# Kernel tuning notes

Measured on AMD Instinct MI355X. Metric: run time of the kernel, lower is better.

Reference implementation:

```python
import jax, jax.numpy as jnp
import numpy as np
from jax import lax
from jax.scipy.special import logsumexp

LOG2PI = 1.8378770664093453

def _gauss_lp(x, mean, logvar):
    return -0.5 * ((x - mean) ** 2 * jnp.exp(-logvar) + logvar + LOG2PI)

def setup_inputs() -> dict:
    key = jax.random.key(0)
    ks = jax.random.split(key, 12)
    B, T, D, H, X, K, U = 32, 1024, 512, 512, 32, 8, 2
    s = 0.05
    return {
        'ys': jax.random.normal(ks[0], (B, T, D), jnp.float32),
        'us': jax.random.normal(ks[1], (B, T, U), jnp.float32),
        'eps': jax.random.normal(ks[2], (B, T, X), jnp.float32),
        'W1': jax.random.normal(ks[3], (D, H), jnp.float32) * s,
        'b1': jnp.zeros((H,), jnp.float32),
        'Wmu': jax.random.normal(ks[4], (H, X), jnp.float32) * s,
        'bmu': jnp.zeros((X,), jnp.float32),
        'Wlv': jax.random.normal(ks[5], (H, X), jnp.float32) * s,
        'blv': jnp.zeros((X,), jnp.float32),
        'Wz': jax.random.normal(ks[6], (X, K * K), jnp.float32) * s,
        'bz': jnp.zeros((K * K,), jnp.float32),
        'A': jax.random.normal(ks[7], (K, X, X), jnp.float32) * s,
        'Bu': jax.random.normal(ks[8], (K, U, X), jnp.float32) * s,
        'bx': jnp.zeros((K, X), jnp.float32),
        'x_logvar': jnp.zeros((K, X), jnp.float32),
        'x0_mean': jax.random.normal(ks[9], (K, X), jnp.float32) * s,
        'x0_logvar': jnp.zeros((K, X), jnp.float32),
        'C': jax.random.normal(ks[10], (X, D), jnp.float32) * s,
        'd': jnp.zeros((D,), jnp.float32),
        'y_logvar': jnp.zeros((D,), jnp.float32),
        'log_init_z': jnp.zeros((K,), jnp.float32),
    }

def _forward_backward(log_a, log_b, log_init):
    # log_a: [B,T,K,K] with log_a[:,t,j,k] = log p(z_t=j | z_{t-1}=k); log_b: [B,T,K]
    B, T, K = log_b.shape
    la = jnp.moveaxis(log_a[:, 1:], 1, 0)  # [T-1,B,K,K]
    lb = jnp.moveaxis(log_b[:, 1:], 1, 0)  # [T-1,B,K]
    a0 = log_init[None, :] + log_b[:, 0]
    c0 = logsumexp(a0, axis=-1)
    a0 = a0 - c0[:, None]
    def fstep(alpha, ab):
        la_t, lb_t = ab
        a = lb_t + logsumexp(la_t + alpha[:, None, :], axis=-1)
        c = logsumexp(a, axis=-1)
        an = a - c[:, None]
        return an, (an, c)
    _, (alphas, cs) = lax.scan(fstep, a0, (la, lb))
    log_px = c0 + jnp.sum(cs, axis=0)  # [B] log marginal likelihood
    fwd = jnp.concatenate([a0[None], alphas], axis=0)  # [T,B,K]
    betaT = jnp.zeros((B, K), log_b.dtype)
    def bstep(beta, ab):
        la_t, lb_t = ab
        b = logsumexp(la_t + (lb_t + beta)[:, :, None], axis=1)  # sum over next-state j
        b = b - logsumexp(b, axis=-1, keepdims=True)
        return b, b
    _, betas = lax.scan(bstep, betaT, (la, lb), reverse=True)
    bwd = jnp.concatenate([betas, betaT[None]], axis=0)  # [T,B,K]
    lg = fwd + bwd
    log_gamma1 = lg - logsumexp(lg, axis=-1, keepdims=True)
    return jnp.moveaxis(log_gamma1, 0, 1), log_px

def reference(ys, us, eps, W1, b1, Wmu, bmu, Wlv, blv, Wz, bz, A, Bu, bx,
              x_logvar, x0_mean, x0_logvar, C, d, y_logvar, log_init_z):
    B, T, D = ys.shape
    K, X = x0_mean.shape
    # inference net q(x|y): per-step MLP producing Gaussian, reparameterized sample
    h = jnp.tanh(ys @ W1 + b1)
    mu = h @ Wmu + bmu
    lv = h @ Wlv + blv
    x = mu + jnp.exp(0.5 * lv) * eps                        # [B,T,X]
    x_entropy = 0.5 * jnp.sum(eps ** 2 + lv + LOG2PI, -1)   # -log q(x^), [B,T]
    # discrete transition log p(z_t | z_{t-1}, x_{t-1}) with log(eye) prepended at t=0
    logits = (x[:, :-1] @ Wz + bz).reshape(B, T - 1, K, K)
    log_a_t = jax.nn.log_softmax(logits, axis=-2)           # normalize_logprob axis=-2
    log_eye = jnp.log(jnp.eye(K, dtype=ys.dtype) + 1e-10)[None, None]
    log_a = jnp.concatenate([jnp.broadcast_to(log_eye, (B, 1, K, K)), log_a_t], axis=1)
    # continuous likelihood log p(x_t | x_{t-1}, u_t, z_t=k) -> [B,T,K]
    log_b0 = jnp.sum(_gauss_lp(x[:, 0, None, :], x0_mean, x0_logvar), -1)  # [B,K]
    means = (jnp.einsum('btd,kde->btke', x[:, :-1], A)
             + jnp.einsum('btu,kue->btke', us[:, 1:], Bu) + bx)            # [B,T-1,K,X]
    log_bt = jnp.sum(_gauss_lp(x[:, 1:, None, :], means, x_logvar), -1)
    log_b = jnp.concatenate([log_b0[:, None], log_bt], axis=1)
    log_init = jax.nn.log_softmax(log_init_z)
    log_gamma1, log_px = _forward_backward(log_a, log_b, log_init)
    # posterior-weighted generated mean mixed over states, then emission
    xt1_gen = jnp.sum(means * jnp.exp(log_gamma1[:, 1:, :, None]), axis=-2)
    x_gen1 = jnp.concatenate([x[:, :1], xt1_gen], axis=1)
    y_mean = x_gen1 @ C + d
    log_py = jnp.sum(_gauss_lp(ys, y_mean, y_logvar), -1)   # [B,T]
    log_p_xy = log_px + jnp.sum(log_py, -1)                 # [B]
    log_qx = jnp.mean(jnp.sum(x_entropy, 1))
    elbo = jnp.mean(log_p_xy) + log_qx
    return elbo
```

## Files before the change

### kernel.cpp

```cpp
#include <hip/hip_runtime.h>
#include <math.h>

#define LOG2PI 1.8378770664093453f

#define NB 32
#define NT 1024
#define ND 512
#define NH 512
#define NX 32
#define NK 8
#define NU 2

#define NCH 93
#define CHL 11

typedef __attribute__((ext_vector_type(8))) short bf16x8;
typedef __attribute__((ext_vector_type(4))) float f32x4;

__device__ __forceinline__ unsigned short f2bf(float f) {
    unsigned u = __float_as_uint(f);
    unsigned r = (u + 0x7FFF + ((u >> 16) & 1)) >> 16;
    return (unsigned short)r;
}

#define DPP_X1 0xB1
#define DPP_X2 0x4E
#define DPP_X3 0x1B
#define DPP_X7 0x141

template <int CTRL>
__device__ __forceinline__ float dppx(float v) {
    return __int_as_float(__builtin_amdgcn_update_dpp(
        0, __float_as_int(v), CTRL, 0xF, 0xF, true));
}

__device__ __forceinline__ float fb_matvec(float4 a0, float4 a1, float v) {
    float p1 = dppx<DPP_X1>(v);
    float p2 = dppx<DPP_X2>(v);
    float p3 = dppx<DPP_X3>(v);
    float p7 = dppx<DPP_X7>(v);
    float p4 = dppx<DPP_X7>(p3);
    float p5 = dppx<DPP_X7>(p2);
    float p6 = dppx<DPP_X7>(p1);
    float c0 = fmaf(a0.y, p1, a0.x * v);
    float c1 = fmaf(a0.w, p3, a0.z * p2);
    float c2 = fmaf(a1.y, p5, a1.x * p4);
    float c3 = fmaf(a1.w, p7, a1.z * p6);
    return (c0 + c1) + (c2 + c3);
}

__device__ __forceinline__ float fb_matvecT(float4 a0, float4 a1, float w) {
    float q0 = a0.x * w;
    float t1 = dppx<DPP_X1>(a0.y * w);
    float t2 = dppx<DPP_X2>(a0.z * w);
    float t3 = dppx<DPP_X3>(a0.w * w);
    float t7 = dppx<DPP_X7>(a1.w * w);
    float t4 = dppx<DPP_X7>(dppx<DPP_X3>(a1.x * w));
    float t5 = dppx<DPP_X7>(dppx<DPP_X2>(a1.y * w));
    float t6 = dppx<DPP_X7>(dppx<DPP_X1>(a1.z * w));
    return ((q0 + t1) + (t2 + t3)) + ((t4 + t5) + (t6 + t7));
}

__device__ __forceinline__ float gsum8(float v) {
    float s = v + dppx<DPP_X1>(v);
    s = s + dppx<DPP_X2>(s);
    s = s + dppx<DPP_X7>(dppx<DPP_X3>(s));
    return s;
}

__device__ __forceinline__ float lse8_high(float v) {
    float m = v;
    m = fmaxf(m, __shfl_xor(m, 8, 64));
    m = fmaxf(m, __shfl_xor(m, 16, 64));
    m = fmaxf(m, __shfl_xor(m, 32, 64));
    float s = expf(v - m);
    s += __shfl_xor(s, 8, 64);
    s += __shfl_xor(s, 16, 64);
    s += __shfl_xor(s, 32, 64);
    return m + logf(s);
}

__global__ __launch_bounds__(256) void k_castT(
    const float* __restrict__ W, unsigned short* __restrict__ WT)
{
    __shared__ float tile[32][33];
    const int bx = blockIdx.x * 32;
    const int by = blockIdx.y * 32;
    const int tx = threadIdx.x & 31, ty = threadIdx.x >> 5;
    for (int i = ty; i < 32; i += 8)
        tile[i][tx] = W[(size_t)(bx + i) * 512 + by + tx];
    __syncthreads();
    for (int i = ty; i < 32; i += 8)
        WT[(size_t)(by + i) * 512 + bx + tx] = f2bf(tile[tx][i]);
}

__global__ __launch_bounds__(256) void k_cast_mulv(
    const float* __restrict__ Wmu, const float* __restrict__ Wlv,
    unsigned short* __restrict__ out)
{
    __shared__ float tile[32][33];
    const float* W = blockIdx.y ? Wlv : Wmu;
    const int base = blockIdx.y * 32;
    const int g = blockIdx.x;
    const int tx = threadIdx.x & 31, ty = threadIdx.x >> 5;
    for (int i = ty; i < 32; i += 8)
        tile[i][tx] = W[(size_t)(g * 32 + i) * 32 + tx];
    __syncthreads();
    for (int i = ty; i < 32; i += 8)
        out[(size_t)(base + i) * 512 + g * 32 + tx] = f2bf(tile[tx][i]);
}

__global__ __launch_bounds__(256) void k_prepc1(
    const float* __restrict__ ylv, float* __restrict__ ivbuf,
    float* __restrict__ term0)
{
    __shared__ float part[256];
    const int tid = threadIdx.x;
    float s = 0.f;
    for (int i = tid; i < 512; i += 256) {
        float lv = ylv[i];
        ivbuf[i] = expf(-lv);
        s += lv + LOG2PI;
    }
    part[tid] = s;
    __syncthreads();
    for (int st = 128; st; st >>= 1) {
        if (tid < st) part[tid] += part[tid + st];
        __syncthreads();
    }
    if (tid == 0) term0[0] = part[0];
}

__global__ __launch_bounds__(256) void k_prepc2(
    const float* __restrict__ C, const float* __restrict__ dvec,
    const float* __restrict__ ivbuf, unsigned short* __restrict__ W2bf,
    float* __restrict__ G, float* __restrict__ c2x)
{
    const int x = blockIdx.x;
    const int tid = threadIdx.x;
    if (x == 32) {
        for (int i = tid; i < 32 * 512; i += 256)
            W2bf[i] = f2bf(C[i] * ivbuf[i & 511]);
        return;
    }
    const int y = tid >> 3, seg = tid & 7;
    const float* Cx = &C[(size_t)x * 512];
    const float* Cy = &C[(size_t)y * 512];
    float p = 0.f;
    for (int j = 0; j < 64; ++j) {
        int dcol = seg * 64 + j;
        p = fmaf(Cx[dcol] * ivbuf[dcol], Cy[dcol], p);
    }
    p = gsum8(p);
    if (seg == 0) G[x * 33 + y] = p;
    if (tid < 8) {
        float q = 0.f;
        for (int j = 0; j < 64; ++j) {
            int dcol = tid * 64 + j;
            q = fmaf(Cx[dcol] * ivbuf[dcol], dvec[dcol], q);
        }
        q = gsum8(q);
        if (tid == 0) c2x[x] = q;
    }
}

__global__ __launch_bounds__(256) void k_gemm_h_mfma(
    const float* __restrict__ ys,
    const unsigned short* __restrict__ Bbf,
    const float* __restrict__ b1, unsigned short* __restrict__ hb)
{
    __shared__ unsigned short As[128 * 64];
    __shared__ unsigned short Bs[128 * 64];
    const int tid = threadIdx.x;
    const int bm = blockIdx.y * 128;
    const int bn = blockIdx.x * 128;
    const int wid = tid >> 6, lane = tid & 63;
    const int wm = wid >> 1, wn = wid & 1;

    f32x4 acc[4][4];
#pragma unroll
    for (int m = 0; m < 4; ++m)
#pragma unroll
        for (int n = 0; n < 4; ++n)
            acc[m][n] = (f32x4){0.f, 0.f, 0.f, 0.f};

    for (int k0 = 0; k0 < 512; k0 += 64) {
#pragma unroll
        for (int r = 0; r < 4; ++r) {
            int l = tid + r * 256;
            int row = l >> 3, c8 = l & 7;
            int sidx = row * 8 + (c8 ^ (row & 7));
            const float4 f0 = *reinterpret_cast<const float4*>(
                &ys[(size_t)(bm + row) * 512 + k0 + c8 * 8]);
            const float4 f1 = *reinterpret_cast<const float4*>(
                &ys[(size_t)(bm + row) * 512 + k0 + c8 * 8 + 4]);
            uint4 ua;
            ua.x = (unsigned)f2bf(f0.x) | ((unsigned)f2bf(f0.y) << 16);
            ua.y = (unsigned)f2bf(f0.z) | ((unsigned)f2bf(f0.w) << 16);
            ua.z = (unsigned)f2bf(f1.x) | ((unsigned)f2bf(f1.y) << 16);
            ua.w = (unsigned)f2bf(f1.z) | ((unsigned)f2bf(f1.w) << 16);
            *reinterpret_cast<uint4*>(&As[sidx * 8]) = ua;
            uint4 vb = *reinterpret_cast<const uint4*>(
                &Bbf[(size_t)(bn + row) * 512 + k0 + c8 * 8]);
            *reinterpret_cast<uint4*>(&Bs[sidx * 8]) = vb;
        }
        __syncthreads();
#pragma unroll
        for (int kh = 0; kh < 2; ++kh) {
            bf16x8 af[4], bfr[4];
            const int c8r = kh * 4 + (lane >> 4);
#pragma unroll
            for (int m = 0; m < 4; ++m) {
                int rA = wm * 64 + m * 16 + (lane & 15);
                af[m] = *reinterpret_cast<bf16x8*>(
                    &As[rA * 64 + (c8r ^ (rA & 7)) * 8]);
            }
#pragma unroll
            for (int n = 0; n < 4; ++n) {
                int rB = wn * 64 + n * 16 + (lane & 15);
                bfr[n] = *reinterpret_cast<bf16x8*>(
                    &Bs[rB * 64 + (c8r ^ (rB & 7)) * 8]);
            }
#pragma unroll
            for (int m = 0; m < 4; ++m)
#pragma unroll
                for (int n = 0; n < 4; ++n)
                    acc[m][n] = __builtin_amdgcn_mfma_f32_16x16x32_bf16(
                        af[m], bfr[n], acc[m][n], 0, 0, 0);
        }
        __syncthreads();
    }
    float b1v[4];
#pragma unroll
    for (int n = 0; n < 4; ++n)
        b1v[n] = b1[bn + wn * 64 + n * 16 + (lane & 15)];
#pragma unroll
    for (int m = 0; m < 4; ++m) {
#pragma unroll
        for (int q = 0; q < 4; ++q) {
            int row = bm + wm * 64 + m * 16 + (lane >> 4) * 4 + q;
#pragma unroll
            for (int n = 0; n < 4; ++n) {
                int col = bn + wn * 64 + n * 16 + (lane & 15);
                hb[(size_t)row * 512 + col] = f2bf(tanhf(acc[m][n][q] + b1v[n]));
            }
        }
    }
}

__global__ __launch_bounds__(256) void k_mulv_mfma(
    const unsigned short* __restrict__ hbf,
    const unsigned short* __restrict__ Wt,
    const float* __restrict__ bmu, const float* __restrict__ blv,
    const float* __restrict__ eps,
    float* __restrict__ x, float* __restrict__ xent)
{
    __shared__ unsigned short As[128 * 64];
    __shared__ unsigned short Bs[64 * 64];
    const int tid = threadIdx.x;
    const int bm = blockIdx.x * 128;
    const int wid = tid >> 6, lane = tid & 63;
    f32x4 acc[2][4];
#pragma unroll
    for (int m = 0; m < 2; ++m)
#pragma unroll
        for (int n = 0; n < 4; ++n)
            acc[m][n] = (f32x4){0.f, 0.f, 0.f, 0.f};

    for (int k0 = 0; k0 < 512; k0 += 64) {
#pragma unroll
        for (int r = 0; r < 4; ++r) {
            int l = tid + r * 256, row = l >> 3, c8 = l & 7;
            int sidx = row * 8 + (c8 ^ (row & 7));
            uint4 v = *reinterpret_cast<const uint4*>(
                &hbf[(size_t)(bm + row) * 512 + k0 + c8 * 8]);
            *reinterpret_cast<uint4*>(&As[sidx * 8]) = v;
        }
#pragma unroll
        for (int r = 0; r < 2; ++r) {
            int l = tid + r * 256, row = l >> 3, c8 = l & 7;
            int sidx = row * 8 + (c8 ^ (row & 7));
            uint4 v = *reinterpret_cast<const uint4*>(
                &Wt[(size_t)row * 512 + k0 + c8 * 8]);
            *reinterpret_cast<uint4*>(&Bs[sidx * 8]) = v;
        }
        __syncthreads();
#pragma unroll
        for (int kh = 0; kh < 2; ++kh) {
            const int c8r = kh * 4 + (lane >> 4);
            bf16x8 af[2], bfr[4];
#pragma unroll
            for (int m = 0; m < 2; ++m) {
                int rA = wid * 32 + m * 16 + (lane & 15);
                af[m] = *reinterpret_cast<bf16x8*>(
                    &As[rA * 64 + (c8r ^ (rA & 7)) * 8]);
            }
#pragma unroll
            for (int n = 0; n < 4; ++n) {
                int rB = n * 16 + (lane & 15);
                bfr[n] = *reinterpret_cast<bf16x8*>(
                    &Bs[rB * 64 + (c8r ^ (rB & 7)) * 8]);
            }
#pragma unroll
            for (int m = 0; m < 2; ++m)
#pragma unroll
                for (int n = 0; n < 4; ++n)
                    acc[m][n] = __builtin_amdgcn_mfma_f32_16x16x32_bf16(
                        af[m], bfr[n], acc[m][n], 0, 0, 0);
        }
        __syncthreads();
    }
    const int o0 = lane & 15, o1 = 16 + (lane & 15);
    const float bm0 = bmu[o0], bm1 = bmu[o1];
    const float bl0 = blv[o0], bl1 = blv[o1];
#pragma unroll
    for (int m = 0; m < 2; ++m) {
#pragma unroll
        for (int q = 0; q < 4; ++q) {
            int row = bm + wid * 32 + m * 16 + (lane >> 4) * 4 + q;
            float mu0 = acc[m][0][q] + bm0;
            float mu1 = acc[m][1][q] + bm1;
            float lv0 = acc[m][2][q] + bl0;
            float lv1 = acc[m][3][q] + bl1;
            float e0 = eps[(size_t)row * 32 + o0];
            float e1 = eps[(size_t)row * 32 + o1];
            x[(size_t)row * 32 + o0] = mu0 + expf(0.5f * lv0) * e0;
            x[(size_t)row * 32 + o1] = mu1 + expf(0.5f * lv1) * e1;
            float pe = (e0 * e0 + lv0) + (e1 * e1 + lv1);
            pe += __shfl_xor(pe, 1, 64);
            pe += __shfl_xor(pe, 2, 64);
            pe += __shfl_xor(pe, 4, 64);
            pe += __shfl_xor(pe, 8, 64);
            if ((lane & 15) == 0)
                xent[row] = 0.5f * (pe + 32.f * LOG2PI);
        }
    }
}

__global__ __launch_bounds__(256) void k_proj(
    const float* __restrict__ ys, const unsigned short* __restrict__ W2bf,
    const float* __restrict__ dvec, const float* __restrict__ ivbuf,
    float* __restrict__ proj, float* __restrict__ term1)
{
    __shared__ unsigned short As[128 * 64];
    __shared__ unsigned short Bs[32 * 64];
    const int tid = threadIdx.x;
    const int bm = blockIdx.x * 128;
    const int wid = tid >> 6, lane = tid & 63;
    const int c8 = tid & 7;
    f32x4 acc[2][2];
#pragma unroll
    for (int m = 0; m < 2; ++m)
#pragma unroll
        for (int n = 0; n < 2; ++n)
            acc[m][n] = (f32x4){0.f, 0.f, 0.f, 0.f};
    float t1p[4] = {0.f, 0.f, 0.f, 0.f};

    for (int k0 = 0; k0 < 512; k0 += 64) {
        const float4 dv0 = *reinterpret_cast<const float4*>(&dvec[k0 + c8 * 8]);
        const float4 dv1 = *reinterpret_cast<const float4*>(&dvec[k0 + c8 * 8 + 4]);
        const float4 iv0 = *reinterpret_cast<const float4*>(&ivbuf[k0 + c8 * 8]);
        const float4 iv1 = *reinterpret_cast<const float4*>(&ivbuf[k0 + c8 * 8 + 4]);
#pragma unroll
        for (int r = 0; r < 4; ++r) {
            int l = tid + r * 256;
            int row = l >> 3;
            int sidx = row * 8 + (c8 ^ (row & 7));
            const float4 f0 = *reinterpret_cast<const float4*>(
                &ys[(size_t)(bm + row) * 512 + k0 + c8 * 8]);
            const float4 f1 = *reinterpret_cast<const float4*>(
                &ys[(size_t)(bm + row) * 512 + k0 + c8 * 8 + 4]);
            float g0 = f0.x - dv0.x, g1 = f0.y - dv0.y;
            float g2 = f0.z - dv0.z, g3 = f0.w - dv0.w;
            float g4 = f1.x - dv1.x, g5 = f1.y - dv1.y;
            float g6 = f1.z - dv1.z, g7 = f1.w - dv1.w;
            t1p[r] += (g0 * g0 * iv0.x + g1 * g1 * iv0.y)
                    + (g2 * g2 * iv0.z + g3 * g3 * iv0.w)
                    + (g4 * g4 * iv1.x + g5 * g5 * iv1.y)
                    + (g6 * g6 * iv1.z + g7 * g7 * iv1.w);
            uint4 ua;
            ua.x = (unsigned)f2bf(f0.x) | ((unsigned)f2bf(f0.y) << 16);
            ua.y = (unsigned)f2bf(f0.z) | ((unsigned)f2bf(f0.w) << 16);
            ua.z = (unsigned)f2bf(f1.x) | ((unsigned)f2bf(f1.y) << 16);
            ua.w = (unsigned)f2bf(f1.z) | ((unsigned)f2bf(f1.w) << 16);
            *reinterpret_cast<uint4*>(&As[sidx * 8]) = ua;
        }
        {
            int row = tid >> 3;
            int sidx = row * 8 + (c8 ^ (row & 7));
            uint4 v = *reinterpret_cast<const uint4*>(
                &W2bf[(size_t)row * 512 + k0 + c8 * 8]);
            *reinterpret_cast<uint4*>(&Bs[sidx * 8]) = v;
        }
        __syncthreads();
#pragma unroll
        for (int kh = 0; kh < 2; ++kh) {
            const int c8r = kh * 4 + (lane >> 4);
            bf16x8 af[2], bfr[2];
#pragma unroll
            for (int m = 0; m < 2; ++m) {
                int rA = wid * 32 + m * 16 + (lane & 15);
                af[m] = *reinterpret_cast<bf16x8*>(
                    &As[rA * 64 + (c8r ^ (rA & 7)) * 8]);
            }
#pragma unroll
            for (int n = 0; n < 2; ++n) {
                int rB = n * 16 + (lane & 15);
                bfr[n] = *reinterpret_cast<bf16x8*>(
                    &Bs[rB * 64 + (c8r ^ (rB & 7)) * 8]);
            }
#pragma unroll
            for (int m = 0; m < 2; ++m)
#pragma unroll
                for (int n = 0; n < 2; ++n)
                    acc[m][n] = __builtin_amdgcn_mfma_f32_16x16x32_bf16(
                        af[m], bfr[n], acc[m][n], 0, 0, 0);
        }
        __syncthreads();
    }
#pragma unroll
    for (int m = 0; m < 2; ++m)
#pragma unroll
        for (int q = 0; q < 4; ++q) {
            int row = bm + wid * 32 + m * 16 + (lane >> 4) * 4 + q;
#pragma unroll
            for (int n = 0; n < 2; ++n) {
                int col = n * 16 + (lane & 15);
                proj[(size_t)row * 32 + col] = acc[m][n][q];
            }
        }
#pragma unroll
    for (int r = 0; r < 4; ++r) {
        float s = gsum8(t1p[r]);
        if ((tid & 7) == 0) term1[bm + (tid >> 3) + r * 32] = s;
    }
}

__global__ __launch_bounds__(256) void k_loga(
    const float* __restrict__ x, const float* __restrict__ Wz,
    const float* __restrict__ bz, float* __restrict__ ap1)
{
    const int tid = threadIdx.x;
    const int item = blockIdx.x * 4 + (tid >> 6);
    const int lane = tid & 63;
    const int t = item & (NT - 1);
    if (t == 0) return;
    const int j = lane >> 3, k = lane & 7;
    const float* xr = &x[((size_t)item - 1) * 32];
    float acc = bz[lane];
#pragma unroll
    for (int e = 0; e < 32; ++e) acc = fmaf(xr[e], Wz[e * 64 + lane], acc);
    float lse = lse8_high(acc);
    ap1[(size_t)item * 64 + j * 8 + (j ^ k)] = expf(acc - lse);
}

__global__ __launch_bounds__(256) void k_means(
    const float* __restrict__ x, const float* __restrict__ us,
    const float* __restrict__ A, const float* __restrict__ Bu,
    const float* __restrict__ bx, const float* __restrict__ x_logvar,
    float* __restrict__ means, float* __restrict__ log_b)
{
    __shared__ float xs[32];
    __shared__ float uu[2];
    const int item = blockIdx.x;
    const int b = item / 1023;
    const int tm = item - b * 1023;
    const int tid = threadIdx.x;
    const int k = tid >> 5, xo = tid & 31;
    if (tid < 32) xs[tid] = x[((size_t)b * NT + tm) * 32 + tid];
    if (tid < 2) uu[tid] = us[((size_t)b * NT + tm + 1) * 2 + tid];
    __syncthreads();
    float acc = bx[k * 32 + xo];
#pragma unroll
    for (int e = 0; e < 32; ++e)
        acc = fmaf(xs[e], A[((size_t)k * 32 + e) * 32 + xo], acc);
    acc = fmaf(uu[0], Bu[((size_t)k * 2 + 0) * 32 + xo], acc);
    acc = fmaf(uu[1], Bu[((size_t)k * 2 + 1) * 32 + xo], acc);
    means[((size_t)item * 8 + k) * 32 + xo] = acc;
    float xv = x[((size_t)b * NT + tm + 1) * 32 + xo];
    float lvv = x_logvar[k * 32 + xo];
    float dd = xv - acc;
    float term = -0.5f * (dd * dd * expf(-lvv) + lvv + LOG2PI);
    for (int m = 16; m; m >>= 1) term += __shfl_down(term, m, 32);
    if (xo == 0) log_b[((size_t)b * NT + tm + 1) * 8 + k] = term;
}

__global__ __launch_bounds__(256) void k_logb0(
    const float* __restrict__ x, const float* __restrict__ x0_mean,
    const float* __restrict__ x0_logvar, float* __restrict__ log_b)
{
    const int b = blockIdx.x;
    const int tid = threadIdx.x;
    const int k = tid >> 5, xo = tid & 31;
    float xv = x[((size_t)b * NT) * 32 + xo];
    float mm = x0_mean[k * 32 + xo];
    float lvv = x0_logvar[k * 32 + xo];
    float dd = xv - mm;
    float term = -0.5f * (dd * dd * expf(-lvv) + lvv + LOG2PI);
    for (int m = 16; m; m >>= 1) term += __shfl_down(term, m, 32);
    if (xo == 0) log_b[(size_t)b * NT * 8 + k] = term;
}

__global__ __launch_bounds__(256) void k_prep(
    const float* __restrict__ log_b, float* __restrict__ bexp,
    float* __restrict__ mbsum)
{
    __shared__ float part[256];
    const int b = blockIdx.x;
    const int tid = threadIdx.x;
    float msum = 0.f;
    for (int t = tid; t < NT; t += 256) {
        const float* lbp = &log_b[((size_t)b * NT + t) * 8];
        float4 l0 = *reinterpret_cast<const float4*>(lbp);
        float4 l1 = *reinterpret_cast<const float4*>(lbp + 4);
        float mm = fmaxf(fmaxf(fmaxf(l0.x, l0.y), fmaxf(l0.z, l0.w)),
                         fmaxf(fmaxf(l1.x, l1.y), fmaxf(l1.z, l1.w)));
        float4 e0, e1;
        e0.x = expf(l0.x - mm); e0.y = expf(l0.y - mm);
        e0.z = expf(l0.z - mm); e0.w = expf(l0.w - mm);
        e1.x = expf(l1.x - mm); e1.y = expf(l1.y - mm);
        e1.z = expf(l1.z - mm); e1.w = expf(l1.w - mm);
        float* bp = &bexp[((size_t)b * NT + t) * 8];
        *reinterpret_cast<float4*>(bp) = e0;
        *reinterpret_cast<float4*>(bp + 4) = e1;
        msum += mm;
    }
    part[tid] = msum;
    __syncthreads();
    for (int s = 128; s; s >>= 1) {
        if (tid < s) part[tid] += part[tid + s];
        __syncthreads();
    }
    if (tid == 0) mbsum[b] = part[0];
}

__global__ __launch_bounds__(256) void k_fbA(
    const float* __restrict__ ap1, const float* __restrict__ bexp,
    float* __restrict__ Pfx, float* __restrict__ sA)
{
    const int tid = threadIdx.x;
    const int wg = blockIdx.x * 4 + (tid >> 6);
    const int lane = tid & 63;
    const int b = wg / NCH;
    const int c = wg - b * NCH;
    const int j = lane >> 3, k = lane & 7;
    const float* ap = &ap1[(size_t)b * NT * 64];
    const float* be = &bexp[(size_t)b * NT * 8];
    int t = CHL * c + 1;
    float P = be[t * 8 + j] * ap[t * 64 + j * 8 + (j ^ k)];
    float sacc = 0.f;
    for (int i = 1; i < CHL; ++i) {
        ++t;
        float4 m0 = *reinterpret_cast<const float4*>(&ap[(size_t)t * 64 + j * 8]);
        float4 m1 = *reinterpret_cast<const float4*>(&ap[(size_t)t * 64 + j * 8 + 4]);
        float bj = be[(size_t)t * 8 + j];
        float x1 = __shfl_xor(P, 8, 64);
        float x2 = __shfl_xor(P, 16, 64);
        float x3 = __shfl_xor(P, 24, 64);
        float x4 = __shfl_xor(P, 32, 64);
        float x5 = __shfl_xor(P, 40, 64);
        float x6 = __shfl_xor(P, 48, 64);
        float x7 = __shfl_xor(P, 56, 64);
        float c0 = fmaf(m0.y, x1, m0.x * P);
        float c1 = fmaf(m0.w, x3, m0.z * x2);
        float c2 = fmaf(m1.y, x5, m1.x * x4);
        float c3 = fmaf(m1.w, x7, m1.z * x6);
        P = bj * ((c0 + c1) + (c2 + c3));
        if ((i & 3) == 3) {
            float mx = P;
            mx = fmaxf(mx, __shfl_xor(mx, 1, 64));
            mx = fmaxf(mx, __shfl_xor(mx, 2, 64));
            mx = fmaxf(mx, __shfl_xor(mx, 4, 64));
            mx = fmaxf(mx, __shfl_xor(mx, 8, 64));
            mx = fmaxf(mx, __shfl_xor(mx, 16, 64));
            mx = fmaxf(mx, __shfl_xor(mx, 32, 64));
            mx = fmaxf(mx, 1e-30f);
            float r = __builtin_amdgcn_rcpf(mx);
            P *= r;
            sacc -= __logf(r);
        }
    }
    Pfx[((size_t)b * NCH + c) * 64 + j * 8 + (j ^ k)] = P;
    if (lane == 0) sA[b * NCH + c] = sacc;
}

__global__ __launch_bounds__(128) void k_fbB(
    const float* __restrict__ Pfx, const float* __restrict__ sA,
    const float* __restrict__ bexp, const float* __restrict__ mbsum,
    const float* __restrict__ log_init_z,
    float* __restrict__ alphaB, float* __restrict__ betaB,
    float* __restrict__ log_px)
{
    const int b = blockIdx.x;
    const int tid = threadIdx.x;
    const int wave = tid >> 6;
    const int lane = tid & 63;
    const int st = lane & 7;
    const float* pf = &Pfx[(size_t)b * NCH * 64];
    if (wave == 0) {
        float liv[8];
        float mz = -1e30f, sz = 0.f;
#pragma unroll
        for (int q = 0; q < 8; ++q) liv[q] = log_init_z[q];
#pragma unroll
        for (int q = 0; q < 8; ++q) mz = fmaxf(mz, liv[q]);
#pragma unroll
        for (int q = 0; q < 8; ++q) sz += expf(liv[q] - mz);
        float alpha = (expf(liv[st] - mz) / sz) * bexp[(size_t)b * NT * 8 + st];
        float logS = 0.f, sAsum = 0.f;
        {
            float s = fmaxf(gsum8(alpha), 1e-35f);
            logS += __logf(s);
            alpha *= __builtin_amdgcn_rcpf(s);
        }
        if (lane < 8) alphaB[((size_t)b * (NCH + 1)) * 8 + lane] = alpha;
        for (int c = 0; c < NCH; ++c) {
            float4 a0 = *reinterpret_cast<const float4*>(&pf[(size_t)c * 64 + st * 8]);
            float4 a1 = *reinterpret_cast<const float4*>(&pf[(size_t)c * 64 + st * 8 + 4]);
            alpha = fb_matvec(a0, a1, alpha);
            float s = fmaxf(gsum8(alpha), 1e-35f);
            logS += __logf(s);
            alpha *= __builtin_amdgcn_rcpf(s);
            sAsum += sA[b * NCH + c];
            if (lane < 8) alphaB[((size_t)b * (NCH + 1) + c + 1) * 8 + lane] = alpha;
        }
        if (lane == 0) log_px[b] = mbsum[b] + sAsum + logS;
    } else {
        float beta = 1.f;
        if (lane < 8) betaB[((size_t)b * (NCH + 1) + NCH) * 8 + lane] = 1.f;
        for (int c = NCH - 1; c >= 0; --c) {
            float4 a0 = *reinterpret_cast<const float4*>(&pf[(size_t)c * 64 + st * 8]);
            float4 a1 = *reinterpret_cast<const float4*>(&pf[(size_t)c * 64 + st * 8 + 4]);
            beta = fb_matvecT(a0, a1, beta);
            float s = fmaxf(gsum8(beta), 1e-35f);
            beta *= __builtin_amdgcn_rcpf(s);
            if (lane < 8) betaB[((size_t)b * (NCH + 1) + c) * 8 + lane] = beta;
        }
    }
}

__global__ __launch_bounds__(256) void k_fbC(
    const float* __restrict__ ap1, const float* __restrict__ bexp,
    const float* __restrict__ alphaB, const float* __restrict__ betaB,
    float* __restrict__ gamma)
{
    __shared__ float alphaS[32][CHL][8];
    const int tid = threadIdx.x;
    const int g = tid >> 3;
    const int st = tid & 7;
    const int task = blockIdx.x * 32 + g;
    const int b = task / NCH;
    const int c = task - b * NCH;
    const float* ap = &ap1[(size_t)b * NT * 64];
    const float* be = &bexp[(size_t)b * NT * 8];
    const int t0 = CHL * c;
    float alpha = alphaB[((size_t)b * (NCH + 1) + c) * 8 + st];
#pragma unroll
    for (int i = 1; i <= CHL; ++i) {
        int t = t0 + i;
        float4 a0 = *reinterpret_cast<const float4*>(&ap[(size_t)t * 64 + st * 8]);
        float4 a1 = *reinterpret_cast<const float4*>(&ap[(size_t)t * 64 + st * 8 + 4]);
        float bv = be[(size_t)t * 8 + st];
        alpha = fb_matvec(a0, a1, alpha) * bv;
        if (i == 5)
            alpha *= __builtin_amdgcn_rcpf(fmaxf(gsum8(alpha), 1e-35f));
        alphaS[g][i - 1][st] = alpha;
    }
    float beta = betaB[((size_t)b * (NCH + 1) + c + 1) * 8 + st];
#pragma unroll
    for (int i = CHL; i >= 1; --i) {
        int t = t0 + i;
        float gv = alphaS[g][i - 1][st] * beta;
        float s = fmaxf(gsum8(gv), 1e-35f);
        gamma[((size_t)b * NT + t) * 8 + st] = gv * __builtin_amdgcn_rcpf(s);
        float4 a0 = *reinterpret_cast<const float4*>(&ap[(size_t)t * 64 + st * 8]);
        float4 a1 = *reinterpret_cast<const float4*>(&ap[(size_t)t * 64 + st * 8 + 4]);
        float bv = be[(size_t)t * 8 + st];
        beta = fb_matvecT(a0, a1, beta * bv);
        if (i == 6)
            beta *= __builtin_amdgcn_rcpf(fmaxf(gsum8(beta), 1e-35f));
    }
    if (c == 0) {
        float a0v = alphaB[((size_t)b * (NCH + 1)) * 8 + st];
        float gv = a0v * beta;
        float s = fmaxf(gsum8(gv), 1e-35f);
        gamma[((size_t)b * NT) * 8 + st] = gv * __builtin_amdgcn_rcpf(s);
    }
}

__global__ __launch_bounds__(256) void k_py(
    const float* __restrict__ x, const float* __restrict__ means,
    const float* __restrict__ gamma, const float* __restrict__ proj,
    const float* __restrict__ term1, const float* __restrict__ Gm,
    const float* __restrict__ c2x, const float* __restrict__ term0,
    const float* __restrict__ xent, float* __restrict__ red)
{
    __shared__ float Gs[32 * 33];
    __shared__ float c2s[32];
    __shared__ float xgS[8][32];
    const int tid = threadIdx.x;
    const int itemBase = blockIdx.x * 8;
    const int b = itemBase >> 10;
    const int t0 = itemBase & (NT - 1);
    for (int i = tid; i < 32 * 33; i += 256) Gs[i] = Gm[i];
    if (tid < 32) c2s[tid] = c2x[tid];
    __syncthreads();
    const int it = tid >> 5;
    const int xo = tid & 31;
    const int t = t0 + it;
    const int item = itemBase + it;
    float xg;
    if (t == 0) {
        xg = x[(size_t)item * 32 + xo];
    } else {
        const float* gp = &gamma[(size_t)item * 8];
        const float* mp = &means[(((size_t)b * 1023 + (t - 1)) * 8) * 32 + xo];
        float4 g0 = *reinterpret_cast<const float4*>(gp);
        float4 g1 = *reinterpret_cast<const float4*>(gp + 4);
        xg = mp[0 * 32] * g0.x;
        xg = fmaf(mp[1 * 32], g0.y, xg);
        xg = fmaf(mp[2 * 32], g0.z, xg);
        xg = fmaf(mp[3 * 32], g0.w, xg);
        xg = fmaf(mp[4 * 32], g1.x, xg);
        xg = fmaf(mp[5 * 32], g1.y, xg);
        xg = fmaf(mp[6 * 32], g1.z, xg);
        xg = fmaf(mp[7 * 32], g1.w, xg);
    }
    xgS[it][xo] = xg;
    __syncthreads();
    float gmv = 0.f;
#pragma unroll 8
    for (int y = 0; y < 32; ++y)
        gmv = fmaf(Gs[xo * 33 + y], xgS[it][y], gmv);
    float val = xg * (proj[(size_t)item * 32 + xo] - c2s[xo] - 0.5f * gmv);
    val += __shfl_xor(val, 1, 64);
    val += __shfl_xor(val, 2, 64);
    val += __shfl_xor(val, 4, 64);
    val += __shfl_xor(val, 8, 64);
    val += __shfl_xor(val, 16, 64);
    if (xo == 0)
        red[item] = -0.5f * (term1[item] + term0[0]) + val + xent[item];
}

__global__ __launch_bounds__(256) void k_final(
    const float* __restrict__ red, const float* __restrict__ log_px,
    float* __restrict__ out)
{
    __shared__ float ssum[4];
    float s = 0.f;
    for (int i = threadIdx.x; i < NB * NT; i += 256) s += red[i];
    if (threadIdx.x < NB) s += log_px[threadIdx.x];
#pragma unroll
    for (int m = 1; m < 64; m <<= 1) s += __shfl_xor(s, m, 64);
    if ((threadIdx.x & 63) == 0) ssum[threadIdx.x >> 6] = s;
    __syncthreads();
    if (threadIdx.x == 0)
        out[0] = (ssum[0] + ssum[1] + ssum[2] + ssum[3]) / (float)NB;
}

extern "C" void kernel_launch(void* const* d_in, const int* in_sizes, int n_in,
                              void* d_out, int out_size, void* d_ws,
                              size_t ws_size, hipStream_t stream)
{
    const float* ys        = (const float*)d_in[0];
    const float* us        = (const float*)d_in[1];
    const float* eps       = (const float*)d_in[2];
    const float* W1        = (const float*)d_in[3];
    const float* b1        = (const float*)d_in[4];
    const float* Wmu       = (const float*)d_in[5];
    const float* bmu       = (const float*)d_in[6];
    const float* Wlv       = (const float*)d_in[7];
    const float* blv       = (const float*)d_in[8];
    const float* Wz        = (const float*)d_in[9];
    const float* bz        = (const float*)d_in[10];
    const float* A         = (const float*)d_in[11];
    const float* Bu        = (const float*)d_in[12];
    const float* bx        = (const float*)d_in[13];
    const float* x_logvar  = (const float*)d_in[14];
    const float* x0_mean   = (const float*)d_in[15];
    const float* x0_logvar = (const float*)d_in[16];
    const float* C         = (const float*)d_in[17];
    const float* dv        = (const float*)d_in[18];
    const float* y_logvar  = (const float*)d_in[19];
    const float* log_init_z= (const float*)d_in[20];
    float* out = (float*)d_out;

    float* ws = (float*)d_ws;
    float* hbf_f  = ws;
    float* x      = hbf_f + 8388608;
    float* xent   = x + 1048576;
    float* ap1    = xent + 32768;
    float* bexp   = ap1 + 2097152;
    float* log_b  = bexp + 262144;
    float* means  = log_b + 262144;
    float* gam    = means + 8380416;
    float* log_px = gam + 262144;
    float* mbsum  = log_px + 32;
    float* red    = mbsum + 32;
    float* w1t_f  = red + 32768;
    float* wmlv_f = w1t_f + 131072;
    float* proj   = wmlv_f + 16384;
    float* term1  = proj + 1048576;
    float* ivbuf  = term1 + 32768;
    float* w2bf_f = ivbuf + 512;
    float* Gm     = w2bf_f + 8192;
    float* c2x    = Gm + 1056;
    float* term0  = c2x + 32;
    float* Pfx    = term0 + 1;
    float* sA     = Pfx + 190464;
    float* alphaB = sA + 2976;
    float* betaB  = alphaB + 24064;

    unsigned short* hbf  = (unsigned short*)hbf_f;
    unsigned short* w1t  = (unsigned short*)w1t_f;
    unsigned short* wmlv = (unsigned short*)wmlv_f;
    unsigned short* w2bf = (unsigned short*)w2bf_f;

    k_castT    <<<dim3(16, 16), 256, 0, stream>>>(W1, w1t);
    k_cast_mulv<<<dim3(16, 2), 256, 0, stream>>>(Wmu, Wlv, wmlv);
    k_prepc1   <<<1, 256, 0, stream>>>(y_logvar, ivbuf, term0);
    k_prepc2   <<<33, 256, 0, stream>>>(C, dv, ivbuf, w2bf, Gm, c2x);
    k_gemm_h_mfma<<<dim3(4, 256), 256, 0, stream>>>(ys, w1t, b1, hbf);
    k_proj     <<<256, 256, 0, stream>>>(ys, w2bf, dv, ivbuf, proj, term1);
    k_mulv_mfma<<<256, 256, 0, stream>>>(hbf, wmlv, bmu, blv, eps, x, xent);
    k_loga <<<8192, 256, 0, stream>>>(x, Wz, bz, ap1);
    k_means<<<32 * 1023, 256, 0, stream>>>(x, us, A, Bu, bx, x_logvar, means, log_b);
    k_logb0<<<32, 256, 0, stream>>>(x, x0_mean, x0_logvar, log_b);
    k_prep <<<32, 256, 0, stream>>>(log_b, bexp, mbsum);
    k_fbA  <<<744, 256, 0, stream>>>(ap1, bexp, Pfx, sA);
    k_fbB  <<<32, 128, 0, stream>>>(Pfx, sA, bexp, mbsum, log_init_z,
                                    alphaB, betaB, log_px);
    k_fbC  <<<93, 256, 0, stream>>>(ap1, bexp, alphaB, betaB, gam);
    k_py   <<<4096, 256, 0, stream>>>(x, means, gam, proj, term1, Gm, c2x,
                                      term0, xent, red);
    k_final<<<1, 256, 0, stream>>>(red, log_px, out);
}
```

Measured before the change: 271.2 us.

## Precast ys to bf16 once, drop means buffer by recomputing in k_py

Adds a kernel that converts ys to bf16 and computes the term1 quadratic in one pass. Both GEMMs then read the compact bf16 copy instead of each re-reading and converting fp32 ys, and the h GEMM grid is swapped so row tiles vary fastest. The ~32MB means tensor is no longer written; k_means now batches 8 items per block with A staged in LDS and k_py recomputes the per-state means from A. This trades extra arithmetic and an extra bf16 write/read of ys for much less global memory traffic.

Result: slower. 283.0 us (+4.4%).

```diff
diff --git a/kernel.cpp b/kernel.cpp
--- a/kernel.cpp
+++ b/kernel.cpp
@@ -21,6 +21,12 @@
     unsigned u = __float_as_uint(f);
     unsigned r = (u + 0x7FFF + ((u >> 16) & 1)) >> 16;
     return (unsigned short)r;
+}
+
+__device__ __forceinline__ unsigned pack_bf2(float a, float b) {
+    unsigned ua = __float_as_uint(a) + 0x8000u;
+    unsigned ub = __float_as_uint(b) + 0x8000u;
+    return __builtin_amdgcn_perm(ub, ua, 0x07060302);
 }
 
 #define DPP_X1 0xB1
@@ -164,16 +170,60 @@
     }
 }
 
+__global__ __launch_bounds__(256) void k_cast_ys_t1(
+    const float* __restrict__ ys, const float* __restrict__ dvec,
+    const float* __restrict__ ivbuf, unsigned short* __restrict__ ysb,
+    float* __restrict__ term1)
+{
+    const int tid = threadIdx.x;
+    const int c8 = tid & 7;
+    const int rbase = blockIdx.x * 128;
+    float t1p[4] = {0.f, 0.f, 0.f, 0.f};
+    for (int k0 = 0; k0 < 512; k0 += 64) {
+        const float4 dv0 = *reinterpret_cast<const float4*>(&dvec[k0 + c8 * 8]);
+        const float4 dv1 = *reinterpret_cast<const float4*>(&dvec[k0 + c8 * 8 + 4]);
+        const float4 iv0 = *reinterpret_cast<const float4*>(&ivbuf[k0 + c8 * 8]);
+        const float4 iv1 = *reinterpret_cast<const float4*>(&ivbuf[k0 + c8 * 8 + 4]);
+#pragma unroll
+        for (int r = 0; r < 4; ++r) {
+            int row = rbase + (tid >> 3) + r * 32;
+            const float4 f0 = *reinterpret_cast<const float4*>(
+                &ys[(size_t)row * 512 + k0 + c8 * 8]);
+            const float4 f1 = *reinterpret_cast<const float4*>(
+                &ys[(size_t)row * 512 + k0 + c8 * 8 + 4]);
+            float g0 = f0.x - dv0.x, g1 = f0.y - dv0.y;
+            float g2 = f0.z - dv0.z, g3 = f0.w - dv0.w;
+            float g4 = f1.x - dv1.x, g5 = f1.y - dv1.y;
+            float g6 = f1.z - dv1.z, g7 = f1.w - dv1.w;
+            t1p[r] += (g0 * g0 * iv0.x + g1 * g1 * iv0.y)
+                    + (g2 * g2 * iv0.z + g3 * g3 * iv0.w)
+                    + (g4 * g4 * iv1.x + g5 * g5 * iv1.y)
+                    + (g6 * g6 * iv1.z + g7 * g7 * iv1.w);
+            uint4 ua;
+            ua.x = pack_bf2(f0.x, f0.y);
+            ua.y = pack_bf2(f0.z, f0.w);
+            ua.z = pack_bf2(f1.x, f1.y);
+            ua.w = pack_bf2(f1.z, f1.w);
+            *reinterpret_cast<uint4*>(&ysb[(size_t)row * 512 + k0 + c8 * 8]) = ua;
+        }
+    }
+#pragma unroll
+    for (int r = 0; r < 4; ++r) {
+        float s = gsum8(t1p[r]);
+        if ((tid & 7) == 0) term1[rbase + (tid >> 3) + r * 32] = s;
+    }
+}
+
 __global__ __launch_bounds__(256) void k_gemm_h_mfma(
-    const float* __restrict__ ys,
+    const unsigned short* __restrict__ Abf,
     const unsigned short* __restrict__ Bbf,
     const float* __restrict__ b1, unsigned short* __restrict__ hb)
 {
     __shared__ unsigned short As[128 * 64];
     __shared__ unsigned short Bs[128 * 64];
     const int tid = threadIdx.x;
-    const int bm = blockIdx.y * 128;
-    const int bn = blockIdx.x * 128;
+    const int bm = blockIdx.x * 128;
+    const int bn = blockIdx.y * 128;
     const int wid = tid >> 6, lane = tid & 63;
     const int wm = wid >> 1, wn = wid & 1;
 
@@ -190,16 +240,9 @@
             int l = tid + r * 256;
             int row = l >> 3, c8 = l & 7;
             int sidx = row * 8 + (c8 ^ (row & 7));
-            const float4 f0 = *reinterpret_cast<const float4*>(
-                &ys[(size_t)(bm + row) * 512 + k0 + c8 * 8]);
-            const float4 f1 = *reinterpret_cast<const float4*>(
-                &ys[(size_t)(bm + row) * 512 + k0 + c8 * 8 + 4]);
-            uint4 ua;
-            ua.x = (unsigned)f2bf(f0.x) | ((unsigned)f2bf(f0.y) << 16);
-            ua.y = (unsigned)f2bf(f0.z) | ((unsigned)f2bf(f0.w) << 16);
-            ua.z = (unsigned)f2bf(f1.x) | ((unsigned)f2bf(f1.y) << 16);
-            ua.w = (unsigned)f2bf(f1.z) | ((unsigned)f2bf(f1.w) << 16);
-            *reinterpret_cast<uint4*>(&As[sidx * 8]) = ua;
+            uint4 va = *reinterpret_cast<const uint4*>(
+                &Abf[(size_t)(bm + row) * 512 + k0 + c8 * 8]);
+            *reinterpret_cast<uint4*>(&As[sidx * 8]) = va;
             uint4 vb = *reinterpret_cast<const uint4*>(
                 &Bbf[(size_t)(bn + row) * 512 + k0 + c8 * 8]);
             *reinterpret_cast<uint4*>(&Bs[sidx * 8]) = vb;
@@ -338,55 +381,32 @@
 }
 
 __global__ __launch_bounds__(256) void k_proj(
-    const float* __restrict__ ys, const unsigned short* __restrict__ W2bf,
-    const float* __restrict__ dvec, const float* __restrict__ ivbuf,
-    float* __restrict__ proj, float* __restrict__ term1)
+    const unsigned short* __restrict__ ysb,
+    const unsigned short* __restrict__ W2bf, float* __restrict__ proj)
 {
     __shared__ unsigned short As[128 * 64];
     __shared__ unsigned short Bs[32 * 64];
     const int tid = threadIdx.x;
     const int bm = blockIdx.x * 128;
     const int wid = tid >> 6, lane = tid & 63;
-    const int c8 = tid & 7;
     f32x4 acc[2][2];
 #pragma unroll
     for (int m = 0; m < 2; ++m)
 #pragma unroll
         for (int n = 0; n < 2; ++n)
             acc[m][n] = (f32x4){0.f, 0.f, 0.f, 0.f};
-    float t1p[4] = {0.f, 0.f, 0.f, 0.f};
 
     for (int k0 = 0; k0 < 512; k0 += 64) {
-        const float4 dv0 = *reinterpret_cast<const float4*>(&dvec[k0 + c8 * 8]);
-        const float4 dv1 = *reinterpret_cast<const float4*>(&dvec[k0 + c8 * 8 + 4]);
-        const float4 iv0 = *reinterpret_cast<const float4*>(&ivbuf[k0 + c8 * 8]);
-        const float4 iv1 = *reinterpret_cast<const float4*>(&ivbuf[k0 + c8 * 8 + 4]);
 #pragma unroll
         for (int r = 0; r < 4; ++r) {
-            int l = tid + r * 256;
-            int row = l >> 3;
+            int l = tid + r * 256, row = l >> 3, c8 = l & 7;
             int sidx = row * 8 + (c8 ^ (row & 7));
-            const float4 f0 = *reinterpret_cast<const float4*>(
-                &ys[(size_t)(bm + row) * 512 + k0 + c8 * 8]);
-            const float4 f1 = *reinterpret_cast<const float4*>(
-                &ys[(size_t)(bm + row) * 512 + k0 + c8 * 8 + 4]);
-            float g0 = f0.x - dv0.x, g1 = f0.y - dv0.y;
-            float g2 = f0.z - dv0.z, g3 = f0.w - dv0.w;
-            float g4 = f1.x - dv1.x, g5 = f1.y - dv1.y;
-            float g6 = f1.z - dv1.z, g7 = f1.w - dv1.w;
-            t1p[r] += (g0 * g0 * iv0.x + g1 * g1 * iv0.y)
-                    + (g2 * g2 * iv0.z + g3 * g3 * iv0.w)
-                    + (g4 * g4 * iv1.x + g5 * g5 * iv1.y)
-                    + (g6 * g6 * iv1.z + g7 * g7 * iv1.w);
-            uint4 ua;
-            ua.x = (unsigned)f2bf(f0.x) | ((unsigned)f2bf(f0.y) << 16);
-            ua.y = (unsigned)f2bf(f0.z) | ((unsigned)f2bf(f0.w) << 16);
-            ua.z = (unsigned)f2bf(f1.x) | ((unsigned)f2bf(f1.y) << 16);
-            ua.w = (unsigned)f2bf(f1.z) | ((unsigned)f2bf(f1.w) << 16);
-            *reinterpret_cast<uint4*>(&As[sidx * 8]) = ua;
+            uint4 v = *reinterpret_cast<const uint4*>(
+                &ysb[(size_t)(bm + row) * 512 + k0 + c8 * 8]);
+            *reinterpret_cast<uint4*>(&As[sidx * 8]) = v;
         }
         {
-            int row = tid >> 3;
+            int row = tid >> 3, c8 = tid & 7;
             int sidx = row * 8 + (c8 ^ (row & 7));
             uint4 v = *reinterpret_cast<const uint4*>(
                 &W2bf[(size_t)row * 512 + k0 + c8 * 8]);
@@ -429,11 +449,6 @@
                 proj[(size_t)row * 32 + col] = acc[m][n][q];
             }
         }
-#pragma unroll
-    for (int r = 0; r < 4; ++r) {
-        float s = gsum8(t1p[r]);
-        if ((tid & 7) == 0) term1[bm + (tid >> 3) + r * 32] = s;
-    }
 }
 
 __global__ __launch_bounds__(256) void k_loga(
@@ -454,35 +469,49 @@
     ap1[(size_t)item * 64 + j * 8 + (j ^ k)] = expf(acc - lse);
 }
 
-__global__ __launch_bounds__(256) void k_means(
+__global__ __launch_bounds__(256) void k_means8(
     const float* __restrict__ x, const float* __restrict__ us,
     const float* __restrict__ A, const float* __restrict__ Bu,
     const float* __restrict__ bx, const float* __restrict__ x_logvar,
-    float* __restrict__ means, float* __restrict__ log_b)
-{
-    __shared__ float xs[32];
-    __shared__ float uu[2];
-    const int item = blockIdx.x;
-    const int b = item / 1023;
-    const int tm = item - b * 1023;
-    const int tid = threadIdx.x;
+    float* __restrict__ log_b)
+{
+    __shared__ float As[8192];
+    __shared__ float xs8[8][32];
+    __shared__ float us8[8][2];
+    const int tid = threadIdx.x;
+    const int base = blockIdx.x * 8;
+    for (int i = tid; i < 2048; i += 256)
+        reinterpret_cast<float4*>(As)[i] =
+            reinterpret_cast<const float4*>(A)[i];
+    {
+        int row = tid >> 5, xo = tid & 31;
+        int item = base + row;
+        int b = item / 1023, tm = item - b * 1023;
+        xs8[row][xo] = x[((size_t)b * NT + tm) * 32 + xo];
+        if (xo < 2) us8[row][xo] = us[((size_t)b * NT + tm + 1) * 2 + xo];
+    }
+    __syncthreads();
     const int k = tid >> 5, xo = tid & 31;
-    if (tid < 32) xs[tid] = x[((size_t)b * NT + tm) * 32 + tid];
-    if (tid < 2) uu[tid] = us[((size_t)b * NT + tm + 1) * 2 + tid];
-    __syncthreads();
-    float acc = bx[k * 32 + xo];
-#pragma unroll
-    for (int e = 0; e < 32; ++e)
-        acc = fmaf(xs[e], A[((size_t)k * 32 + e) * 32 + xo], acc);
-    acc = fmaf(uu[0], Bu[((size_t)k * 2 + 0) * 32 + xo], acc);
-    acc = fmaf(uu[1], Bu[((size_t)k * 2 + 1) * 32 + xo], acc);
-    means[((size_t)item * 8 + k) * 32 + xo] = acc;
-    float xv = x[((size_t)b * NT + tm + 1) * 32 + xo];
-    float lvv = x_logvar[k * 32 + xo];
-    float dd = xv - acc;
-    float term = -0.5f * (dd * dd * expf(-lvv) + lvv + LOG2PI);
-    for (int m = 16; m; m >>= 1) term += __shfl_down(term, m, 32);
-    if (xo == 0) log_b[((size_t)b * NT + tm + 1) * 8 + k] = term;
+    const float bxv = bx[k * 32 + xo];
+    const float bu0 = Bu[(k * 2 + 0) * 32 + xo];
+    const float bu1 = Bu[(k * 2 + 1) * 32 + xo];
+    const float lvv = x_logvar[k * 32 + xo];
+    const float ivv = expf(-lvv);
+    const float basev = lvv + LOG2PI;
+    for (int i = 0; i < 8; ++i) {
+        int item = base + i;
+        int b = item / 1023, tm = item - b * 1023;
+        float acc = fmaf(us8[i][0], bu0, fmaf(us8[i][1], bu1, bxv));
+#pragma unroll 8
+        for (int e = 0; e < 32; ++e)
+            acc = fmaf(xs8[i][e], As[k * 1024 + e * 32 + xo], acc);
+        float xv = x[((size_t)b * NT + tm + 1) * 32 + xo];
+        float dd = xv - acc;
+        float term = dd * dd * ivv + basev;
+        for (int m = 16; m; m >>= 1) term += __shfl_down(term, m, 32);
+        if (xo == 0)
+            log_b[((size_t)b * NT + tm + 1) * 8 + k] = -0.5f * term;
+    }
 }
 
 __global__ __launch_bounds__(256) void k_logb0(
@@ -689,21 +718,37 @@
 }
 
 __global__ __launch_bounds__(256) void k_py(
-    const float* __restrict__ x, const float* __restrict__ means,
-    const float* __restrict__ gamma, const float* __restrict__ proj,
-    const float* __restrict__ term1, const float* __restrict__ Gm,
-    const float* __restrict__ c2x, const float* __restrict__ term0,
-    const float* __restrict__ xent, float* __restrict__ red)
-{
+    const float* __restrict__ x, const float* __restrict__ us,
+    const float* __restrict__ A, const float* __restrict__ Bu,
+    const float* __restrict__ bx, const float* __restrict__ gamma,
+    const float* __restrict__ proj, const float* __restrict__ term1,
+    const float* __restrict__ Gm, const float* __restrict__ c2x,
+    const float* __restrict__ term0, const float* __restrict__ xent,
+    float* __restrict__ red)
+{
+    __shared__ float As[8192];
     __shared__ float Gs[32 * 33];
     __shared__ float c2s[32];
+    __shared__ float xp8[8][32];
+    __shared__ float gs[8][8];
+    __shared__ float us8[8][2];
     __shared__ float xgS[8][32];
     const int tid = threadIdx.x;
     const int itemBase = blockIdx.x * 8;
-    const int b = itemBase >> 10;
     const int t0 = itemBase & (NT - 1);
+    for (int i = tid; i < 2048; i += 256)
+        reinterpret_cast<float4*>(As)[i] =
+            reinterpret_cast<const float4*>(A)[i];
     for (int i = tid; i < 32 * 33; i += 256) Gs[i] = Gm[i];
     if (tid < 32) c2s[tid] = c2x[tid];
+    {
+        int it = tid >> 5, xo = tid & 31;
+        int t = t0 + it;
+        int item = itemBase + it;
+        xp8[it][xo] = (t > 0) ? x[((size_t)item - 1) * 32 + xo] : 0.f;
+        if (xo < 8) gs[it][xo] = (t > 0) ? gamma[(size_t)item * 8 + xo] : 0.f;
+        if (xo < 2) us8[it][xo] = (t > 0) ? us[(size_t)item * 2 + xo] : 0.f;
+    }
     __syncthreads();
     const int it = tid >> 5;
     const int xo = tid & 31;
@@ -713,18 +758,17 @@
     if (t == 0) {
         xg = x[(size_t)item * 32 + xo];
     } else {
-        const float* gp = &gamma[(size_t)item * 8];
-        const float* mp = &means[(((size_t)b * 1023 + (t - 1)) * 8) * 32 + xo];
-        float4 g0 = *reinterpret_cast<const float4*>(gp);
-        float4 g1 = *reinterpret_cast<const float4*>(gp + 4);
-        xg = mp[0 * 32] * g0.x;
-        xg = fmaf(mp[1 * 32], g0.y, xg);
-        xg = fmaf(mp[2 * 32], g0.z, xg);
-        xg = fmaf(mp[3 * 32], g0.w, xg);
-        xg = fmaf(mp[4 * 32], g1.x, xg);
-        xg = fmaf(mp[5 * 32], g1.y, xg);
-        xg = fmaf(mp[6 * 32], g1.z, xg);
-        xg = fmaf(mp[7 * 32], g1.w, xg);
+        xg = 0.f;
+#pragma unroll
+        for (int k = 0; k < 8; ++k) {
+            float acc = bx[k * 32 + xo];
+            acc = fmaf(us8[it][0], Bu[(k * 2 + 0) * 32 + xo], acc);
+            acc = fmaf(us8[it][1], Bu[(k * 2 + 1) * 32 + xo], acc);
+#pragma unroll 8
+            for (int e = 0; e < 32; ++e)
+                acc = fmaf(xp8[it][e], As[k * 1024 + e * 32 + xo], acc);
+            xg = fmaf(gs[it][k], acc, xg);
+        }
     }
     xgS[it][xo] = xg;
     __syncthreads();
@@ -792,8 +836,8 @@
     float* ap1    = xent + 32768;
     float* bexp   = ap1 + 2097152;
     float* log_b  = bexp + 262144;
-    float* means  = log_b + 262144;
-    float* gam    = means + 8380416;
+    float* ysb_f  = log_b + 262144;
+    float* gam    = ysb_f + 8388608;
     float* log_px = gam + 262144;
     float* mbsum  = log_px + 32;
     float* red    = mbsum + 32;
@@ -812,26 +856,28 @@
     float* betaB  = alphaB + 24064;
 
     unsigned short* hbf  = (unsigned short*)hbf_f;
+    unsigned short* ysb  = (unsigned short*)ysb_f;
     unsigned short* w1t  = (unsigned short*)w1t_f;
     unsigned short* wmlv = (unsigned short*)wmlv_f;
     unsigned short* w2bf = (unsigned short*)w2bf_f;
 
+    k_prepc1   <<<1, 256, 0, stream>>>(y_logvar, ivbuf, term0);
+    k_cast_ys_t1<<<256, 256, 0, stream>>>(ys, dv, ivbuf, ysb, term1);
     k_castT    <<<dim3(16, 16), 256, 0, stream>>>(W1, w1t);
     k_cast_mulv<<<dim3(16, 2), 256, 0, stream>>>(Wmu, Wlv, wmlv);
-    k_prepc1   <<<1, 256, 0, stream>>>(y_logvar, ivbuf, term0);
     k_prepc2   <<<33, 256, 0, stream>>>(C, dv, ivbuf, w2bf, Gm, c2x);
-    k_gemm_h_mfma<<<dim3(4, 256), 256, 0, stream>>>(ys, w1t, b1, hbf);
-    k_proj     <<<256, 256, 0, stream>>>(ys, w2bf, dv, ivbuf, proj, term1);
+    k_gemm_h_mfma<<<dim3(256, 4), 256, 0, stream>>>(ysb, w1t, b1, hbf);
+    k_proj     <<<256, 256, 0, stream>>>(ysb, w2bf, proj);
     k_mulv_mfma<<<256, 256, 0, stream>>>(hbf, wmlv, bmu, blv, eps, x, xent);
-    k_loga <<<8192, 256, 0, stream>>>(x, Wz, bz, ap1);
-    k_means<<<32 * 1023, 256, 0, stream>>>(x, us, A, Bu, bx, x_logvar, means, log_b);
-    k_logb0<<<32, 256, 0, stream>>>(x, x0_mean, x0_logvar, log_b);
-    k_prep <<<32, 256, 0, stream>>>(log_b, bexp, mbsum);
-    k_fbA  <<<744, 256, 0, stream>>>(ap1, bexp, Pfx, sA);
-    k_fbB  <<<32, 128, 0, stream>>>(Pfx, sA, bexp, mbsum, log_init_z,
-                                    alphaB, betaB, log_px);
-    k_fbC  <<<93, 256, 0, stream>>>(ap1, bexp, alphaB, betaB, gam);
-    k_py   <<<4096, 256, 0, stream>>>(x, means, gam, proj, term1, Gm, c2x,
-                                      term0, xent, red);
-    k_final<<<1, 256, 0, stream>>>(red, log_px, out);
-}
+    k_loga     <<<8192, 256, 0, stream>>>(x, Wz, bz, ap1);
+    k_means8   <<<4092, 256, 0, stream>>>(x, us, A, Bu, bx, x_logvar, log_b);
+    k_logb0    <<<32, 256, 0, stream>>>(x, x0_mean, x0_logvar, log_b);
+    k_prep     <<<32, 256, 0, stream>>>(log_b, bexp, mbsum);
+    k_fbA      <<<744, 256, 0, stream>>>(ap1, bexp, Pfx, sA);
+    k_fbB      <<<32, 128, 0, stream>>>(Pfx, sA, bexp, mbsum, log_init_z,
+                                        alphaB, betaB, log_px);
+    k_fbC      <<<93, 256, 0, stream>>>(ap1, bexp, alphaB, betaB, gam);
+    k_py       <<<4096, 256, 0, stream>>>(x, us, A, Bu, bx, gam, proj, term1,
+                                          Gm, c2x, term0, xent, red);
+    k_final    <<<1, 256, 0, stream>>>(red, log_px, out);
+}
```
